# Kernel optimization log

Measured on AMD Instinct MI355X. Metric: run time of the kernel, lower is better.

## Reference

```python
import jax, jax.numpy as jnp
import numpy as np

D_MODEL = 1024
N_HEADS = 16
D_HEAD = D_MODEL // N_HEADS
QLEN = 512
MLEN = 512
BATCH = 8


def setup_inputs() -> dict:
    key = jax.random.key(0)
    ks = jax.random.split(key, 12)
    s = 0.02
    inputs = jax.random.normal(ks[0], (QLEN, BATCH, D_MODEL), jnp.float32)
    r = jax.random.normal(ks[1], (QLEN + MLEN, 1, D_MODEL), jnp.float32)
    u = jax.random.normal(ks[2], (N_HEADS, D_HEAD), jnp.float32) * s
    v = jax.random.normal(ks[3], (N_HEADS, D_HEAD), jnp.float32) * s
    mem = jax.random.normal(ks[4], (MLEN, BATCH, D_MODEL), jnp.float32)
    # attention params (Transformer-XL style): fused qkv, r-projection, output proj
    W_qkv = jax.random.normal(ks[5], (D_MODEL, 3 * D_MODEL), jnp.float32) * s
    W_r = jax.random.normal(ks[6], (D_MODEL, D_MODEL), jnp.float32) * s
    W_o = jax.random.normal(ks[7], (D_MODEL, D_MODEL), jnp.float32) * s
    # GRU params: input-hidden and hidden-hidden for gates (r, z, n), torch layout
    W_ih = jax.random.normal(ks[8], (3 * D_MODEL, D_MODEL), jnp.float32) * s
    W_hh = jax.random.normal(ks[9], (3 * D_MODEL, D_MODEL), jnp.float32) * s
    b_ih = jax.random.normal(ks[10], (3 * D_MODEL,), jnp.float32) * s
    b_hh = jax.random.normal(ks[11], (3 * D_MODEL,), jnp.float32) * s
    h0 = jnp.zeros((BATCH, D_MODEL), jnp.float32)
    return dict(inputs=inputs, r=r, u=u, v=v, mem=mem, W_qkv=W_qkv, W_r=W_r,
                W_o=W_o, W_ih=W_ih, W_hh=W_hh, b_ih=b_ih, b_hh=b_hh, h0=h0)


def _rel_shift(x):
    # x: [q, k, b, h] -> Transformer-XL relative shift
    q, k, b, h = x.shape
    zero_pad = jnp.zeros((q, 1, b, h), x.dtype)
    x_padded = jnp.concatenate([zero_pad, x], axis=1)        # [q, k+1, b, h]
    x_padded = x_padded.reshape(k + 1, q, b, h)
    return x_padded[1:].reshape(q, k, b, h)


def _attention(inputs, r, u, v, mem, W_qkv, W_r, W_o):
    qlen, bsz, _ = inputs.shape
    cat = jnp.concatenate([mem, inputs], axis=0)             # [klen, b, d]
    klen = cat.shape[0]
    qkv = cat @ W_qkv                                        # [klen, b, 3d]
    w_head_q, w_head_k, w_head_v = jnp.split(qkv, 3, axis=-1)
    w_head_q = w_head_q[-qlen:]                              # [q, b, d]
    r_head_k = (r[:, 0, :] @ W_r).reshape(klen, N_HEADS, D_HEAD)  # [k, h, dh]

    q_ = w_head_q.reshape(qlen, bsz, N_HEADS, D_HEAD)
    k_ = w_head_k.reshape(klen, bsz, N_HEADS, D_HEAD)
    v_ = w_head_v.reshape(klen, bsz, N_HEADS, D_HEAD)

    AC = jnp.einsum('ibhd,jbhd->ijbh', q_ + u[None, None], k_)
    BD = jnp.einsum('ibhd,jhd->ijbh', q_ + v[None, None], r_head_k)
    BD = _rel_shift(BD)
    scale = 1.0 / np.sqrt(D_HEAD)
    attn_score = (AC + BD) * scale                           # [q, k, b, h]

    # causal mask with memory: query i attends to keys j <= i + mlen
    mlen = klen - qlen
    i = jnp.arange(qlen)[:, None]
    j = jnp.arange(klen)[None, :]
    mask = j > (i + mlen)                                    # [q, k]
    attn_score = jnp.where(mask[:, :, None, None], -jnp.inf, attn_score)

    attn_prob = jax.nn.softmax(attn_score, axis=1)
    attn_vec = jnp.einsum('ijbh,jbhd->ibhd', attn_prob, v_)
    attn_vec = attn_vec.reshape(qlen, bsz, D_MODEL)
    return attn_vec @ W_o                                    # [q, b, d]


def _gru(x, h0, W_ih, W_hh, b_ih, b_hh):
    # x: [T, B, D]; torch GRU cell math
    Wi_r, Wi_z, Wi_n = jnp.split(W_ih, 3, axis=0)
    Wh_r, Wh_z, Wh_n = jnp.split(W_hh, 3, axis=0)
    bi_r, bi_z, bi_n = jnp.split(b_ih, 3)
    bh_r, bh_z, bh_n = jnp.split(b_hh, 3)

    # precompute input projections for all timesteps
    xr = x @ Wi_r.T + bi_r
    xz = x @ Wi_z.T + bi_z
    xn = x @ Wi_n.T + bi_n

    def step(h, xs):
        xr_t, xz_t, xn_t = xs
        r = jax.nn.sigmoid(xr_t + h @ Wh_r.T + bh_r)
        z = jax.nn.sigmoid(xz_t + h @ Wh_z.T + bh_z)
        n = jnp.tanh(xn_t + r * (h @ Wh_n.T + bh_n))
        h_new = (1.0 - z) * n + z * h
        return h_new, h_new

    _, ys = jax.lax.scan(step, h0, (xr, xz, xn))
    return ys                                                # [T, B, D]


def reference(inputs, r, u, v, mem, W_qkv, W_r, W_o, W_ih, W_hh, b_ih, b_hh, h0):
    y = _attention(inputs, r, u, v, mem, W_qkv, W_r, W_o)
    return _gru(y, h0, W_ih, W_hh, b_ih, b_hh)
```

## Files before the change

### kernel.cpp

```cpp
#include <hip/hip_runtime.h>
#include <math.h>


typedef short bf16x8 __attribute__((ext_vector_type(8)));
typedef float f32x4 __attribute__((ext_vector_type(4)));

union FragU { uint4 u; bf16x8 h; };

__device__ inline void split2(float x0, float x1, unsigned& hi, unsigned& lo) {
    unsigned u0 = __float_as_uint(x0), u1 = __float_as_uint(x1);
    float h0 = __uint_as_float(u0 & 0xffff0000u);
    float h1 = __uint_as_float(u1 & 0xffff0000u);
    unsigned l0 = __float_as_uint(x0 - h0), l1 = __float_as_uint(x1 - h1);
    hi = (u0 >> 16) | (u1 & 0xffff0000u);
    lo = (l0 >> 16) | (l1 & 0xffff0000u);
}

__device__ __forceinline__ void gl_lds16(const uint4* g, uint4* l) {
    __builtin_amdgcn_global_load_lds(
        (const __attribute__((address_space(1))) uint4*)g,
        (__attribute__((address_space(3))) uint4*)l, 16, 0, 0);
}

template<bool TR>
__global__ __launch_bounds__(256) void prep_w(
    const float* __restrict__ W, unsigned* __restrict__ out, int Nr, int K, int ldw)
{
    int idx = blockIdx.x * 256 + threadIdx.x;
    int cpr = K >> 3;
    if (idx >= Nr * cpr) return;
    int n, c;
    if (TR) { n = idx % Nr; c = idx / Nr; }
    else    { c = idx % cpr; n = idx / cpr; }
    int kt = c >> 2, j = c & 3;
    int k = kt * 32 + j * 8;
    float x[8];
    #pragma unroll
    for (int i = 0; i < 8; ++i)
        x[i] = TR ? W[(size_t)(k + i) * ldw + n] : W[(size_t)n * ldw + k + i];
    unsigned h[4], l[4];
    split2(x[0], x[1], h[0], l[0]);
    split2(x[2], x[3], h[1], l[1]);
    split2(x[4], x[5], h[2], l[2]);
    split2(x[6], x[7], h[3], l[3]);
    unsigned* base = out + (size_t)n * K + kt * 32;
    *(uint4*)(base + (((2 * j) ^ (n & 7)) * 4))     = make_uint4(h[0], h[1], h[2], h[3]);
    *(uint4*)(base + (((2 * j + 1) ^ (n & 7)) * 4)) = make_uint4(l[0], l[1], l[2], l[3]);
}

template<int AMODE, bool BIAS>
__global__ __launch_bounds__(256) void gemm_mfma(
    const float* __restrict__ A, const float* __restrict__ A2,
    const unsigned* __restrict__ Bp, const float* __restrict__ bias,
    float* __restrict__ C, int M, int N, int K, int lda, int ldc)
{
    __shared__ uint4 Ab[1024];
    __shared__ uint4 Bb[1024];
    int tid = threadIdx.x;
    int lane = tid & 63, wid = tid >> 6;
    int wr = wid >> 1, wc = wid & 1;
    int n0 = blockIdx.x * 128, m0 = blockIdx.y * 128;
    int r15 = lane & 15, s = lane >> 4;

    f32x4 acc[4][4];
    #pragma unroll
    for (int i = 0; i < 4; ++i)
        #pragma unroll
        for (int j = 0; j < 4; ++j) acc[i][j] = 0.0f;

    for (int kt = 0; kt < (K >> 5); ++kt) {
        int k0 = kt * 32;
        #pragma unroll
        for (int q = 0; q < 2; ++q) {
            int idx = q * 256 + tid;
            int row = idx >> 2, j = idx & 3;
            const float* ap;
            if (AMODE == 1) {
                int gm = m0 + row;
                ap = (gm < 4096) ? (A + (size_t)gm * lda) : (A2 + (size_t)(gm - 4096) * lda);
            } else {
                ap = A + (size_t)(m0 + row) * lda;
            }
            float4 x0 = *(const float4*)(ap + k0 + j * 8);
            float4 x1 = *(const float4*)(ap + k0 + j * 8 + 4);
            unsigned h[4], l[4];
            split2(x0.x, x0.y, h[0], l[0]);
            split2(x0.z, x0.w, h[1], l[1]);
            split2(x1.x, x1.y, h[2], l[2]);
            split2(x1.z, x1.w, h[3], l[3]);
            Ab[row * 8 + (((2 * j) ^ (row & 7)))]     = make_uint4(h[0], h[1], h[2], h[3]);
            Ab[row * 8 + (((2 * j + 1) ^ (row & 7)))] = make_uint4(l[0], l[1], l[2], l[3]);
        }
        #pragma unroll
        for (int q = 0; q < 4; ++q) {
            int idx = q * 256 + tid;
            int row = idx >> 3, slot = idx & 7;
            Bb[idx] = *(const uint4*)(Bp + (size_t)(n0 + row) * K + k0 + slot * 4);
        }
        __syncthreads();
        FragU ahi[4], alo[4], bhi[4], blo[4];
        #pragma unroll
        for (int f = 0; f < 4; ++f) {
            int ar = wr * 64 + f * 16 + r15;
            ahi[f].u = Ab[ar * 8 + ((2 * s) ^ (ar & 7))];
            alo[f].u = Ab[ar * 8 + ((2 * s + 1) ^ (ar & 7))];
            int br = wc * 64 + f * 16 + r15;
            bhi[f].u = Bb[br * 8 + ((2 * s) ^ (br & 7))];
            blo[f].u = Bb[br * 8 + ((2 * s + 1) ^ (br & 7))];
        }
        #pragma unroll
        for (int fi = 0; fi < 4; ++fi)
            #pragma unroll
            for (int fj = 0; fj < 4; ++fj) {
                acc[fi][fj] = __builtin_amdgcn_mfma_f32_16x16x32_bf16(ahi[fi].h, bhi[fj].h, acc[fi][fj], 0, 0, 0);
                acc[fi][fj] = __builtin_amdgcn_mfma_f32_16x16x32_bf16(ahi[fi].h, blo[fj].h, acc[fi][fj], 0, 0, 0);
                acc[fi][fj] = __builtin_amdgcn_mfma_f32_16x16x32_bf16(alo[fi].h, bhi[fj].h, acc[fi][fj], 0, 0, 0);
            }
        __syncthreads();
    }
    int r4 = (lane >> 4) * 4;
    #pragma unroll
    for (int fj = 0; fj < 4; ++fj) {
        int n = n0 + wc * 64 + fj * 16 + r15;
        float bv = BIAS ? bias[n] : 0.f;
        #pragma unroll
        for (int fi = 0; fi < 4; ++fi) {
            int m = m0 + wr * 64 + fi * 16 + r4;
            #pragma unroll
            for (int r = 0; r < 4; ++r)
                C[(size_t)(m + r) * ldc + n] = acc[fi][fj][r] + bv;
        }
    }
}

__global__ __launch_bounds__(256) void attn_fused(
    const float* __restrict__ qkv, const float* __restrict__ rk,
    const float* __restrict__ u_, const float* __restrict__ v_,
    float* __restrict__ y1)
{
    __shared__ float qu[64][68], qv[64][68], Kt[64][68], Vt[64][68];
    __shared__ float RKs[128][68];
    __shared__ float S[64][68];
    __shared__ float mrow[64], lrow[64], scalef[64];
    __shared__ float pmax[64][16], psum[64][16];

    int tid = threadIdx.x;
    int it = blockIdx.x, b = blockIdx.y, h = blockIdx.z;
    int i0 = it * 64;
    int ti = tid >> 4, tj = tid & 15;

    {
        int r = tid >> 2, c0 = (tid & 3) * 16;
        size_t base = ((size_t)(i0 + r + 512) * 8 + b) * 3072 + h * 64;
        #pragma unroll
        for (int q = 0; q < 4; ++q) {
            int c = c0 + q * 4;
            float4 qq = *(const float4*)&qkv[base + c];
            float4 uu = *(const float4*)&u_[h * 64 + c];
            float4 vv = *(const float4*)&v_[h * 64 + c];
            *(float4*)&qu[r][c] = make_float4(qq.x + uu.x, qq.y + uu.y, qq.z + uu.z, qq.w + uu.w);
            *(float4*)&qv[r][c] = make_float4(qq.x + vv.x, qq.y + vv.y, qq.z + vv.z, qq.w + vv.w);
        }
    }
    if (tid < 64) { mrow[tid] = -1e30f; lrow[tid] = 0.f; }

    float Od[4][4] = {};
    int njt = it + 9;

    for (int jt = 0; jt < njt; ++jt) {
        int j0 = jt * 64;
        __syncthreads();
        {
            int r = tid >> 2, c0 = (tid & 3) * 16;
            size_t kb = ((size_t)(j0 + r) * 8 + b) * 3072 + 1024 + h * 64;
            #pragma unroll
            for (int q = 0; q < 4; ++q) {
                int c = c0 + q * 4;
                *(float4*)&Kt[r][c] = *(const float4*)&qkv[kb + c];
                *(float4*)&Vt[r][c] = *(const float4*)&qkv[kb + 1024 + c];
            }
        }
        {
            int r2 = tid >> 1, c0 = (tid & 1) * 32;
            int jj = j0 - i0 + 448 + r2;
            jj = jj < 0 ? 0 : (jj > 1023 ? 1023 : jj);
            size_t rb = (size_t)jj * 1024 + h * 64;
            #pragma unroll
            for (int q = 0; q < 8; ++q) {
                int c = c0 + q * 4;
                *(float4*)&RKs[r2][c] = *(const float4*)&rk[rb + c];
            }
        }
        __syncthreads();

        float acc[4][4] = {};
        int jlb = (tj - ti) * 4 + 60;
        #pragma unroll 4
        for (int d4 = 0; d4 < 64; d4 += 4) {
            float4 Aq[4], Cq[4], Kv[4], Rv[7];
            #pragma unroll
            for (int i = 0; i < 4; ++i) {
                Aq[i] = *(float4*)&qu[ti * 4 + i][d4];
                Cq[i] = *(float4*)&qv[ti * 4 + i][d4];
                Kv[i] = *(float4*)&Kt[tj * 4 + i][d4];
            }
            #pragma unroll
            for (int t = 0; t < 7; ++t)
                Rv[t] = *(float4*)&RKs[jlb + t][d4];
            #pragma unroll
            for (int i = 0; i < 4; ++i)
                #pragma unroll
                for (int j = 0; j < 4; ++j) {
                    float4 kk = Kv[j];
                    float4 rr = Rv[j - i + 3];
                    acc[i][j] += Aq[i].x * kk.x + Aq[i].y * kk.y + Aq[i].z * kk.z + Aq[i].w * kk.w
                               + Cq[i].x * rr.x + Cq[i].y * rr.y + Cq[i].z * rr.z + Cq[i].w * rr.w;
                }
        }
        #pragma unroll
        for (int i = 0; i < 4; ++i) {
            int gi = i0 + ti * 4 + i;
            float mx = -1e30f;
            #pragma unroll
            for (int j = 0; j < 4; ++j) {
                int gj = j0 + tj * 4 + j;
                float vS = acc[i][j] * 0.125f;
                if (gj > gi + 512) vS = -1e30f;
                acc[i][j] = vS;
                mx = fmaxf(mx, vS);
            }
            pmax[ti * 4 + i][tj] = mx;
        }
        __syncthreads();
        if (tid < 64) {
            float mo = mrow[tid], mn = mo;
            #pragma unroll
            for (int t = 0; t < 16; ++t) mn = fmaxf(mn, pmax[tid][t]);
            mrow[tid] = mn;
            scalef[tid] = __expf(mo - mn);
        }
        __syncthreads();
        #pragma unroll
        for (int i = 0; i < 4; ++i) {
            int ri = ti * 4 + i;
            float mn = mrow[ri];
            float4 pv;
            pv.x = __expf(acc[i][0] - mn);
            pv.y = __expf(acc[i][1] - mn);
            pv.z = __expf(acc[i][2] - mn);
            pv.w = __expf(acc[i][3] - mn);
            *(float4*)&S[ri][tj * 4] = pv;
            psum[ri][tj] = pv.x + pv.y + pv.z + pv.w;
            float scl = scalef[ri];
            #pragma unroll
            for (int j2 = 0; j2 < 4; ++j2) Od[i][j2] *= scl;
        }
        __syncthreads();
        if (tid < 64) {
            float s = 0.f;
            #pragma unroll
            for (int t = 0; t < 16; ++t) s += psum[tid][t];
            lrow[tid] = lrow[tid] * scalef[tid] + s;
        }
        #pragma unroll 4
        for (int jb = 0; jb < 64; jb += 4) {
            float4 p0 = *(float4*)&S[ti * 4 + 0][jb];
            float4 p1 = *(float4*)&S[ti * 4 + 1][jb];
            float4 p2 = *(float4*)&S[ti * 4 + 2][jb];
            float4 p3 = *(float4*)&S[ti * 4 + 3][jb];
            float4 v0 = *(float4*)&Vt[jb + 0][tj * 4];
            float4 v1 = *(float4*)&Vt[jb + 1][tj * 4];
            float4 v2 = *(float4*)&Vt[jb + 2][tj * 4];
            float4 v3 = *(float4*)&Vt[jb + 3][tj * 4];
            float4 pr[4] = {p0, p1, p2, p3};
            #pragma unroll
            for (int i = 0; i < 4; ++i) {
                Od[i][0] += pr[i].x * v0.x + pr[i].y * v1.x + pr[i].z * v2.x + pr[i].w * v3.x;
                Od[i][1] += pr[i].x * v0.y + pr[i].y * v1.y + pr[i].z * v2.y + pr[i].w * v3.y;
                Od[i][2] += pr[i].x * v0.z + pr[i].y * v1.z + pr[i].z * v2.z + pr[i].w * v3.z;
                Od[i][3] += pr[i].x * v0.w + pr[i].y * v1.w + pr[i].z * v2.w + pr[i].w * v3.w;
            }
        }
    }
    __syncthreads();
    #pragma unroll
    for (int i = 0; i < 4; ++i) {
        int ri = ti * 4 + i;
        float inv = 1.f / lrow[ri];
        float4 o = make_float4(Od[i][0] * inv, Od[i][1] * inv, Od[i][2] * inv, Od[i][3] * inv);
        *(float4*)&y1[((size_t)(i0 + ri) * 8 + b) * 1024 + h * 64 + tj * 4] = o;
    }
}

__global__ __launch_bounds__(256) void prep_whh(
    const float* __restrict__ Whh, uint4* __restrict__ outp)
{
    int idx = blockIdx.x * 256 + threadIdx.x;
    if (idx >= 393216) return;
    int lane = idx & 63;
    int rest = idx >> 6;
    int gate = rest % 3;
    int kt   = (rest / 3) & 31;
    int g64  = rest / 96;
    int n = gate * 1024 + g64 * 16 + (lane & 15);
    int k = kt * 32 + (lane >> 4) * 8;
    const float* src = Whh + (size_t)n * 1024 + k;
    float4 x0 = *(const float4*)src, x1 = *(const float4*)(src + 4);
    unsigned h[4], l[4];
    split2(x0.x, x0.y, h[0], l[0]);
    split2(x0.z, x0.w, h[1], l[1]);
    split2(x1.x, x1.y, h[2], l[2]);
    split2(x1.z, x1.w, h[3], l[3]);
    outp[((size_t)rest * 2 + 0) * 64 + lane] = make_uint4(h[0], h[1], h[2], h[3]);
    outp[((size_t)rest * 2 + 1) * 64 + lane] = make_uint4(l[0], l[1], l[2], l[3]);
}

__global__ __launch_bounds__(256) void gru_step_mfma(
    const float* __restrict__ hin, float* __restrict__ hout,
    const uint4* __restrict__ WhhG, const float* __restrict__ bhh,
    const float* __restrict__ xg, float* __restrict__ out, int t)
{
    __shared__ uint4 Bf[4096];
    __shared__ uint4 Wst[2][1536];
    __shared__ float red[3][64][4];
    int tid = threadIdx.x;
    int lane = tid & 63, wv = tid >> 6;
    int g64 = blockIdx.x;

    int col = lane & 15;
    int d0 = g64 * 16 + (lane >> 4) * 4;
    bool act = (wv == 0) && (col < 8);
    float4 xr4, xz4, xn4, hp4, br4, bz4, bn4;
    if (act) {
        size_t xb = ((size_t)t * 8 + col) * 3072 + d0;
        xr4 = *(const float4*)&xg[xb];
        xz4 = *(const float4*)&xg[xb + 1024];
        xn4 = *(const float4*)&xg[xb + 2048];
        hp4 = *(const float4*)&hin[col * 1024 + d0];
        br4 = *(const float4*)&bhh[d0];
        bz4 = *(const float4*)&bhh[1024 + d0];
        bn4 = *(const float4*)&bhh[2048 + d0];
    }

    for (int s = tid; s < 1024; s += 256) {
        int b = s & 7, oct = (s >> 3) & 3, kt = s >> 5;
        const float* hp = hin + b * 1024 + kt * 32 + oct * 8;
        float4 x0 = *(const float4*)hp, x1 = *(const float4*)(hp + 4);
        unsigned hh[4], ll[4];
        split2(x0.x, x0.y, hh[0], ll[0]);
        split2(x0.z, x0.w, hh[1], ll[1]);
        split2(x1.x, x1.y, hh[2], ll[2]);
        split2(x1.z, x1.w, hh[3], ll[3]);
        int ln = oct * 16 + b;
        Bf[(kt * 2 + 0) * 64 + ln] = make_uint4(hh[0], hh[1], hh[2], hh[3]);
        Bf[(kt * 2 + 1) * 64 + ln] = make_uint4(ll[0], ll[1], ll[2], ll[3]);
    }

    const uint4* wbase = WhhG + (size_t)g64 * 12288;

    #pragma unroll
    for (int i = 0; i < 6; ++i) {
        int slot = (i * 4 + wv) * 64;
        gl_lds16(wbase + slot + lane, &Wst[0][slot]);
    }
    __syncthreads();

    f32x4 acc = 0.0f;
    for (int c = 0; c < 8; ++c) {
        if (c < 7) {
            const uint4* src = wbase + (c + 1) * 1536;
            uint4* dst = &Wst[(c + 1) & 1][0];
            #pragma unroll
            for (int i = 0; i < 6; ++i) {
                int slot = (i * 4 + wv) * 64;
                gl_lds16(src + slot + lane, dst + slot);
            }
        }
        if (wv < 3) {
            const uint4* Wc = &Wst[c & 1][0];
            #pragma unroll
            for (int ktL = 0; ktL < 4; ++ktL) {
                int kt = c * 4 + ktL;
                FragU ah, al, bh, bl;
                ah.u = Wc[((ktL * 3 + wv) * 2 + 0) * 64 + lane];
                al.u = Wc[((ktL * 3 + wv) * 2 + 1) * 64 + lane];
                bh.u = Bf[(kt * 2 + 0) * 64 + lane];
                bl.u = Bf[(kt * 2 + 1) * 64 + lane];
                acc = __builtin_amdgcn_mfma_f32_16x16x32_bf16(ah.h, bh.h, acc, 0, 0, 0);
                acc = __builtin_amdgcn_mfma_f32_16x16x32_bf16(ah.h, bl.h, acc, 0, 0, 0);
                acc = __builtin_amdgcn_mfma_f32_16x16x32_bf16(al.h, bh.h, acc, 0, 0, 0);
            }
        }
        __syncthreads();
    }
    if (wv < 3) *(f32x4*)&red[wv][lane][0] = acc;
    __syncthreads();

    if (act) {
        f32x4 aR = *(f32x4*)&red[0][lane][0];
        f32x4 aZ = *(f32x4*)&red[1][lane][0];
        f32x4 aN = *(f32x4*)&red[2][lane][0];
        float xr[4] = {xr4.x, xr4.y, xr4.z, xr4.w};
        float xz[4] = {xz4.x, xz4.y, xz4.z, xz4.w};
        float xn[4] = {xn4.x, xn4.y, xn4.z, xn4.w};
        float hp[4] = {hp4.x, hp4.y, hp4.z, hp4.w};
        float br[4] = {br4.x, br4.y, br4.z, br4.w};
        float bz[4] = {bz4.x, bz4.y, bz4.z, bz4.w};
        float bn[4] = {bn4.x, bn4.y, bn4.z, bn4.w};
        float hn[4];
        #pragma unroll
        for (int r = 0; r < 4; ++r) {
            float rr = 1.f / (1.f + __expf(-(xr[r] + aR[r] + br[r])));
            float zz = 1.f / (1.f + __expf(-(xz[r] + aZ[r] + bz[r])));
            float nn = tanhf(xn[r] + rr * (aN[r] + bn[r]));
            hn[r] = (1.f - zz) * nn + zz * hp[r];
        }
        float4 hv = make_float4(hn[0], hn[1], hn[2], hn[3]);
        *(float4*)&hout[col * 1024 + d0] = hv;
        *(float4*)&out[((size_t)t * 8 + col) * 1024 + d0] = hv;
    }
}

extern "C" void kernel_launch(void* const* d_in, const int* in_sizes, int n_in,
                              void* d_out, int out_size, void* d_ws, size_t ws_size,
                              hipStream_t stream) {
    (void)in_sizes; (void)n_in; (void)out_size; (void)ws_size;
    const float* inputs = (const float*)d_in[0];
    const float* r_in   = (const float*)d_in[1];
    const float* u_in   = (const float*)d_in[2];
    const float* v_in   = (const float*)d_in[3];
    const float* mem    = (const float*)d_in[4];
    const float* Wqkv   = (const float*)d_in[5];
    const float* Wr     = (const float*)d_in[6];
    const float* Wo     = (const float*)d_in[7];
    const float* Wih    = (const float*)d_in[8];
    const float* Whh    = (const float*)d_in[9];
    const float* bih    = (const float*)d_in[10];
    const float* bhh    = (const float*)d_in[11];
    const float* h0     = (const float*)d_in[12];
    float* out = (float*)d_out;
    float* ws = (float*)d_ws;

    float*    qkv   = ws;
    float*    rk    = ws + 25165824;
    float*    y1    = ws + 26214400;
    float*    y2    = ws + 30408704;
    float*    xg    = ws + 34603008;
    float*    hA    = ws + 47185920;
    float*    hB    = ws + 47194112;
    unsigned* WqkvP = (unsigned*)(ws + 47202304);
    unsigned* WrP   = (unsigned*)(ws + 50348032);
    unsigned* WoP   = (unsigned*)(ws + 51396608);
    unsigned* WihP  = (unsigned*)(ws + 52445184);
    uint4*    WhhG  = (uint4*)qkv;

    dim3 blk(256);
    prep_w<true ><<<1536, blk, 0, stream>>>(Wqkv, WqkvP, 3072, 1024, 3072);
    prep_w<true ><<< 512, blk, 0, stream>>>(Wr,   WrP,   1024, 1024, 1024);
    prep_w<true ><<< 512, blk, 0, stream>>>(Wo,   WoP,   1024, 1024, 1024);
    prep_w<false><<<1536, blk, 0, stream>>>(Wih,  WihP,  3072, 1024, 1024);

    gemm_mfma<1, false><<<dim3(24, 64), blk, 0, stream>>>(
        mem, inputs, WqkvP, nullptr, qkv, 8192, 3072, 1024, 1024, 3072);
    gemm_mfma<0, false><<<dim3(8, 8), blk, 0, stream>>>(
        r_in, nullptr, WrP, nullptr, rk, 1024, 1024, 1024, 1024, 1024);
    attn_fused<<<dim3(8, 8, 16), blk, 0, stream>>>(qkv, rk, u_in, v_in, y1);
    prep_whh<<<1536, blk, 0, stream>>>(Whh, WhhG);
    gemm_mfma<0, false><<<dim3(8, 32), blk, 0, stream>>>(
        y1, nullptr, WoP, nullptr, y2, 4096, 1024, 1024, 1024, 1024);
    gemm_mfma<0, true><<<dim3(24, 32), blk, 0, stream>>>(
        y2, nullptr, WihP, bih, xg, 4096, 3072, 1024, 1024, 3072);

    const float* hin = h0;
    for (int s = 0; s < 512; ++s) {
        float* hp = (s & 1) ? hB : hA;
        gru_step_mfma<<<64, blk, 0, stream>>>(hin, hp, WhhG, bhh, xg, out, s);
        hin = hp;
    }
}
```

Measured before the change: 5.321 ms.

## Replace per-step GRU launches with a persistent cooperative kernel using flag barriers

```diff
diff --git a/kernel.cpp b/kernel.cpp
--- a/kernel.cpp
+++ b/kernel.cpp
@@ -357,7 +357,6 @@
     }
 
     const uint4* wbase = WhhG + (size_t)g64 * 12288;
-
     #pragma unroll
     for (int i = 0; i < 6; ++i) {
         int slot = (i * 4 + wv) * 64;
@@ -418,6 +417,108 @@
         float4 hv = make_float4(hn[0], hn[1], hn[2], hn[3]);
         *(float4*)&hout[col * 1024 + d0] = hv;
         *(float4*)&out[((size_t)t * 8 + col) * 1024 + d0] = hv;
+    }
+}
+
+__global__ __launch_bounds__(512) void gru_persistent(
+    const float* __restrict__ h0, float* __restrict__ hA, float* __restrict__ hB,
+    const float* __restrict__ Whh, const float* __restrict__ bhh,
+    const float* __restrict__ xg, float* __restrict__ out,
+    unsigned* __restrict__ flags)
+{
+    int lane = threadIdx.x & 63;
+    int wave = threadIdx.x >> 6;
+    int d = blockIdx.x * 8 + wave;
+    int kb = lane << 4;
+
+    float4 wgt[3][4];
+    #pragma unroll
+    for (int g = 0; g < 3; ++g)
+        #pragma unroll
+        for (int q = 0; q < 4; ++q)
+            wgt[g][q] = *(const float4*)&Whh[(size_t)(g * 1024 + d) * 1024 + kb + q * 4];
+    float b_r = bhh[d], b_z = bhh[1024 + d], b_n = bhh[2048 + d];
+
+    for (int t = 0; t < 512; ++t) {
+        const float* hi_ = (t == 0) ? h0 : ((t & 1) ? hA : hB);
+        float* ho = (t & 1) ? hB : hA;
+
+        float xr = 0.f, xz = 0.f, xn = 0.f, hprev = 0.f;
+        if (lane < 8) {
+            size_t xb = ((size_t)t * 8 + lane) * 3072 + d;
+            xr = xg[xb];
+            xz = xg[xb + 1024];
+            xn = xg[xb + 2048];
+            hprev = hi_[lane * 1024 + d];
+        }
+
+        float acc[3][8];
+        #pragma unroll
+        for (int g = 0; g < 3; ++g)
+            #pragma unroll
+            for (int b = 0; b < 8; ++b) acc[g][b] = 0.f;
+
+        #pragma unroll
+        for (int b = 0; b < 8; ++b) {
+            const float* hb = hi_ + b * 1024 + kb;
+            float4 h0v = *(const float4*)(hb);
+            float4 h1v = *(const float4*)(hb + 4);
+            float4 h2v = *(const float4*)(hb + 8);
+            float4 h3v = *(const float4*)(hb + 12);
+            #pragma unroll
+            for (int g = 0; g < 3; ++g) {
+                acc[g][b] += wgt[g][0].x * h0v.x + wgt[g][0].y * h0v.y + wgt[g][0].z * h0v.z + wgt[g][0].w * h0v.w
+                           + wgt[g][1].x * h1v.x + wgt[g][1].y * h1v.y + wgt[g][1].z * h1v.z + wgt[g][1].w * h1v.w
+                           + wgt[g][2].x * h2v.x + wgt[g][2].y * h2v.y + wgt[g][2].z * h2v.z + wgt[g][2].w * h2v.w
+                           + wgt[g][3].x * h3v.x + wgt[g][3].y * h3v.y + wgt[g][3].z * h3v.z + wgt[g][3].w * h3v.w;
+            }
+        }
+        #pragma unroll
+        for (int g = 0; g < 3; ++g)
+            #pragma unroll
+            for (int b = 0; b < 8; ++b) {
+                float v = acc[g][b];
+                v += __shfl_xor(v, 32);
+                v += __shfl_xor(v, 16);
+                v += __shfl_xor(v, 8);
+                v += __shfl_xor(v, 4);
+                v += __shfl_xor(v, 2);
+                v += __shfl_xor(v, 1);
+                acc[g][b] = v;
+            }
+
+        if (lane < 8) {
+            float s0 = acc[0][0], s1 = acc[1][0], s2 = acc[2][0];
+            #pragma unroll
+            for (int b = 1; b < 8; ++b)
+                if (lane == b) { s0 = acc[0][b]; s1 = acc[1][b]; s2 = acc[2][b]; }
+            float rr = 1.f / (1.f + __expf(-(xr + s0 + b_r)));
+            float zz = 1.f / (1.f + __expf(-(xz + s1 + b_z)));
+            float nn = tanhf(xn + rr * (s2 + b_n));
+            float hn = (1.f - zz) * nn + zz * hprev;
+            __hip_atomic_store(&ho[lane * 1024 + d], hn, __ATOMIC_RELAXED,
+                               __HIP_MEMORY_SCOPE_AGENT);
+            out[((size_t)t * 8 + lane) * 1024 + d] = hn;
+        }
+
+        if (t != 511) {
+            __syncthreads();
+            unsigned tgt = (unsigned)t + 1u;
+            if (threadIdx.x < 64) {
+                if (threadIdx.x == 0)
+                    __hip_atomic_store(&flags[(size_t)blockIdx.x * 16], tgt,
+                                       __ATOMIC_RELEASE, __HIP_MEMORY_SCOPE_AGENT);
+                const unsigned* f0 = &flags[(size_t)lane * 16];
+                const unsigned* f1 = &flags[(size_t)(lane + 64) * 16];
+                for (;;) {
+                    unsigned a = __hip_atomic_load(f0, __ATOMIC_RELAXED, __HIP_MEMORY_SCOPE_AGENT);
+                    unsigned b = __hip_atomic_load(f1, __ATOMIC_RELAXED, __HIP_MEMORY_SCOPE_AGENT);
+                    if (__all(a >= tgt && b >= tgt)) break;
+                }
+            }
+            __syncthreads();
+            asm volatile("buffer_inv sc1" ::: "memory");
+        }
     }
 }
 
@@ -452,6 +553,7 @@
     unsigned* WrP   = (unsigned*)(ws + 50348032);
     unsigned* WoP   = (unsigned*)(ws + 51396608);
     unsigned* WihP  = (unsigned*)(ws + 52445184);
+    unsigned* flags = (unsigned*)(ws + 55590912);
     uint4*    WhhG  = (uint4*)qkv;
 
     dim3 blk(256);
@@ -459,22 +561,33 @@
     prep_w<true ><<< 512, blk, 0, stream>>>(Wr,   WrP,   1024, 1024, 1024);
     prep_w<true ><<< 512, blk, 0, stream>>>(Wo,   WoP,   1024, 1024, 1024);
     prep_w<false><<<1536, blk, 0, stream>>>(Wih,  WihP,  3072, 1024, 1024);
+    hipMemsetAsync(flags, 0, 8192, stream);
 
     gemm_mfma<1, false><<<dim3(24, 64), blk, 0, stream>>>(
         mem, inputs, WqkvP, nullptr, qkv, 8192, 3072, 1024, 1024, 3072);
     gemm_mfma<0, false><<<dim3(8, 8), blk, 0, stream>>>(
         r_in, nullptr, WrP, nullptr, rk, 1024, 1024, 1024, 1024, 1024);
     attn_fused<<<dim3(8, 8, 16), blk, 0, stream>>>(qkv, rk, u_in, v_in, y1);
-    prep_whh<<<1536, blk, 0, stream>>>(Whh, WhhG);
+    prep_whh<<<1536, blk, 0, stream>>>(Whh, (uint4*)WhhG);
     gemm_mfma<0, false><<<dim3(8, 32), blk, 0, stream>>>(
         y1, nullptr, WoP, nullptr, y2, 4096, 1024, 1024, 1024, 1024);
     gemm_mfma<0, true><<<dim3(24, 32), blk, 0, stream>>>(
         y2, nullptr, WihP, bih, xg, 4096, 3072, 1024, 1024, 3072);
 
-    const float* hin = h0;
-    for (int s = 0; s < 512; ++s) {
-        float* hp = (s & 1) ? hB : hA;
-        gru_step_mfma<<<64, blk, 0, stream>>>(hin, hp, WhhG, bhh, xg, out, s);
-        hin = hp;
-    }
-}
+    {
+        const float* a0 = h0; float* a1 = hA; float* a2 = hB;
+        const float* a3 = Whh; const float* a4 = bhh; const float* a5 = xg;
+        float* a6 = out; unsigned* a7 = flags;
+        void* args[8] = {&a0, &a1, &a2, &a3, &a4, &a5, &a6, &a7};
+        hipError_t e = hipLaunchCooperativeKernel((void*)gru_persistent,
+                                                  dim3(128), dim3(512), args, 0, stream);
+        if (e != hipSuccess) {
+            const float* hin = h0;
+            for (int s = 0; s < 512; ++s) {
+                float* hp = (s & 1) ? hB : hA;
+                gru_step_mfma<<<64, blk, 0, stream>>>(hin, hp, (uint4*)WhhG, bhh, xg, out, s);
+                hin = hp;
+            }
+        }
+    }
+}
```

New measurement: 10.58 ms. 1.99x slower.
